# Performance work log

Hardware: AMD Instinct MI355X
Metric: run time of the kernel (lower is better)

The kernel has to match this reference:

```python
import jax, jax.numpy as jnp
import numpy as np

B, N, C, H = 64, 500, 128, 256
EPS = 1e-5


def _bn(x, g, b):
    # BatchNorm1d in training mode: biased batch statistics
    m = jnp.mean(x, axis=0)
    v = jnp.mean((x - m) ** 2, axis=0)
    return g * (x - m) * jax.lax.rsqrt(v + EPS) + b


def _lin(x, w, b):
    return x @ w.T + b


def setup_inputs() -> dict:
    key = jax.random.key(0)
    ks = jax.random.split(key, 16)

    def w(k, shape, s=0.05):
        return (s * jax.random.normal(k, shape)).astype(jnp.float32)

    return {
        'l2_xyz': jax.random.uniform(ks[0], (B, 3, N), dtype=jnp.float32),
        'l2_points': jax.random.normal(ks[1], (B, C, N), dtype=jnp.float32),
        'l3_points': jax.random.normal(ks[2], (B, C), dtype=jnp.float32),
        'temp': jax.random.uniform(ks[3], (B, 1, N), dtype=jnp.float32) * 400.0,
        'fc_res0_w': w(ks[4], (H, H)), 'fc_res0_b': jnp.zeros((H,), jnp.float32),
        'bn_res0_g': jnp.ones((H,), jnp.float32), 'bn_res0_b': jnp.zeros((H,), jnp.float32),
        'fc_res1_w': w(ks[5], (H, H)), 'fc_res1_b': jnp.zeros((H,), jnp.float32),
        'bn_res1_g': jnp.ones((H,), jnp.float32), 'bn_res1_b': jnp.zeros((H,), jnp.float32),
        'fc_res2_w': w(ks[6], (H, H)), 'fc_res2_b': jnp.zeros((H,), jnp.float32),
        'bn_res2_g': jnp.ones((H,), jnp.float32), 'bn_res2_b': jnp.zeros((H,), jnp.float32),
        'fc_lt1_w': w(ks[7], (H, H)), 'fc_lt1_b': jnp.zeros((H,), jnp.float32),
        'bn_lt1_g': jnp.ones((H,), jnp.float32), 'bn_lt1_b': jnp.zeros((H,), jnp.float32),
        'fc_lt4_w': w(ks[8], (1, H)), 'fc_lt4_b': jnp.zeros((1,), jnp.float32),
    }


def reference(l2_xyz, l2_points, l3_points, temp,
              fc_res0_w, fc_res0_b, bn_res0_g, bn_res0_b,
              fc_res1_w, fc_res1_b, bn_res1_g, bn_res1_b,
              fc_res2_w, fc_res2_b, bn_res2_g, bn_res2_b,
              fc_lt1_w, fc_lt1_b, bn_lt1_g, bn_lt1_b,
              fc_lt4_w, fc_lt4_b):
    point = jnp.transpose(l2_xyz, (0, 2, 1))    # [B,N,3]
    data = jnp.transpose(l2_points, (0, 2, 1))  # [B,N,C]

    # square_distance(point, point), then abs + sqrt
    s = jnp.sum(point * point, axis=-1)  # [B,N]
    sq = s[:, :, None] + s[:, None, :] - 2.0 * jnp.einsum('bik,bjk->bij', point, point)
    dist = jnp.sqrt(jnp.abs(sq))  # [B,N,N]

    # distance-band edge set as a mask (torch.where -> variable edge list)
    mask = ((dist > 0.19) & (dist < 0.21)).astype(data.dtype)  # [B,N,N]
    counts = jnp.maximum(jnp.sum(mask, axis=(1, 2)), 1.0)      # [B] edges per batch

    # per-channel average of data[b,i,c]*data[b,j,c] over edges (b,i,j).
    # Identical math to the torch take/index_add channel loop over corr_matrix,
    # without materializing the [B,C,N,N] outer-product tensor.
    t = jnp.einsum('bij,bjc->bic', mask, data)                  # [B,N,C]
    correlation = jnp.einsum('bic,bic->bc', t, data) / counts[:, None]  # [B,C]

    sa4 = l3_points.reshape(B, C)
    c = jnp.concatenate([correlation, sa4], axis=1)  # [B,256]

    h = jax.nn.relu(_bn(_lin(c, fc_res0_w, fc_res0_b), bn_res0_g, bn_res0_b))
    h = jax.nn.relu(_bn(_lin(h, fc_res1_w, fc_res1_b), bn_res1_g, bn_res1_b))
    h = jax.nn.relu(_bn(_lin(h, fc_res2_w, fc_res2_b), bn_res2_g, bn_res2_b))
    h = jax.nn.relu(_bn(_lin(h, fc_lt1_w, fc_lt1_b), bn_lt1_g, bn_lt1_b))
    tc = _lin(h, fc_lt4_w, fc_lt4_b).squeeze(-1)  # [B]

    tsys = jnp.mean(temp, axis=2).squeeze(-1)     # [B]
    return (tc, tsys, l2_points, correlation)
```

## Files before the change

### kernel.cpp

```cpp
#include <hip/hip_runtime.h>

#define NB 64
#define NP 500
#define NC 128
#define NH 256
#define EPS_BN 1e-5f

#define SEGS 8
#define CAPE 1024

#define EDGE_OFF 0
#define CNT_OFF (NB * SEGS * CAPE)
#define CT_OFF (CNT_OFF + 512)

#define OUT_PTS_OFF 128
#define OUT_CORR_OFF 4096128
#define TOTAL_F4 1024000

#define SCAN_BLKS 512
#define MISC_END 576
#define K1_COPY 1024
#define K1_GRID (MISC_END + K1_COPY)

typedef __attribute__((ext_vector_type(8))) short short8b;
typedef __attribute__((ext_vector_type(4))) float f32x4;

__device__ __forceinline__ short bfh(float f) {
  return (short)(__builtin_bit_cast(unsigned, f) >> 16);
}
__device__ __forceinline__ float bff(short h) {
  return __builtin_bit_cast(float, ((unsigned)(unsigned short)h) << 16);
}

__global__ __launch_bounds__(256) void k1_scan_misc_copy(
    const float* __restrict__ xyz,
    const float* __restrict__ temp,
    const float* __restrict__ l3,
    const float* __restrict__ pts,
    float* __restrict__ out,
    float* __restrict__ ws) {
  const int blk = blockIdx.x;
  const int tid = threadIdx.x;

  if (blk < SCAN_BLKS) {
    const int b = blk >> 3;
    const int jt = blk & 7;
    __shared__ float4 pt[NP];
    __shared__ int lcnt;
    if (tid == 0) lcnt = 0;
    const float* xr = xyz + b * 1500;
    for (int idx = tid; idx < NP; idx += 256) {
      float x = xr[idx], y = xr[500 + idx], z = xr[1000 + idx];
      pt[idx] = make_float4(x, y, z, x * x + y * y + z * z);
    }
    __syncthreads();

    const int j0 = jt * 63;
    const int j1 = (j0 + 63 < NP) ? j0 + 63 : NP;
    const int i0 = tid;
    const int i1 = tid + 256;
    float4 p0 = pt[i0];
    float4 p1 = (i1 < NP) ? pt[i1] : make_float4(0.f, 0.f, 0.f, 0.f);
    int* eseg = (int*)ws + EDGE_OFF + (b * SEGS + jt) * CAPE;

    for (int j = j0; j < j1; ++j) {
      float4 q = pt[j];
      if (i0 < j) {
        float sq = p0.w + q.w - 2.f * (p0.x * q.x + p0.y * q.y + p0.z * q.z);
        float d = sqrtf(fabsf(sq));
        if (d > 0.19f && d < 0.21f) {
          int e = atomicAdd(&lcnt, 1);
          if (e < CAPE) eseg[e] = (i0 << 16) | j;
        }
      }
      if (i1 < j) {
        float sq = p1.w + q.w - 2.f * (p1.x * q.x + p1.y * q.y + p1.z * q.z);
        float d = sqrtf(fabsf(sq));
        if (d > 0.19f && d < 0.21f) {
          int e = atomicAdd(&lcnt, 1);
          if (e < CAPE) eseg[e] = (i1 << 16) | j;
        }
      }
    }
    __syncthreads();
    if (tid == 0) {
      int c = lcnt < CAPE ? lcnt : CAPE;
      ((int*)ws)[CNT_OFF + b * SEGS + jt] = c;
    }
  } else if (blk < MISC_END) {
    const int b = blk - SCAN_BLKS;
    float sum = 0.f;
    for (int i = tid; i < NP; i += 256) sum += temp[b * NP + i];
    for (int off = 32; off; off >>= 1) sum += __shfl_xor(sum, off);
    __shared__ float wsum[4];
    if ((tid & 63) == 0) wsum[tid >> 6] = sum;
    __syncthreads();
    if (tid == 0)
      out[64 + b] = (wsum[0] + wsum[1] + wsum[2] + wsum[3]) * (1.f / 500.f);
    if (tid < NC) ws[CT_OFF + (NC + tid) * 64 + b] = l3[b * NC + tid];
  } else {
    const int cb = blk - MISC_END;
    const float4* src = (const float4*)pts;
    float4* dst = (float4*)(out + OUT_PTS_OFF);
    for (int idx = cb * 256 + tid; idx < TOTAL_F4; idx += K1_COPY * 256)
      dst[idx] = src[idx];
  }
}

__global__ __launch_bounds__(256) void k2_corr(
    const float* __restrict__ data,
    float* __restrict__ out,
    float* __restrict__ ws) {
  const int blk = blockIdx.x;
  const int tid = threadIdx.x;
  const int b = blk >> 3;
  const int c0 = (blk & 7) * 16;
  __shared__ float dT[NP * 20];
  __shared__ float corrp[16];
  if (tid < 16) corrp[tid] = 0.f;

  const float4* in4 = (const float4*)(data + (size_t)b * 64000 + c0 * 500);
  for (int idx = tid; idx < 2000; idx += 256) {
    float4 v = in4[idx];
    int c = idx / 125;
    int j = (idx - c * 125) * 4;
    dT[(j + 0) * 20 + c] = v.x;
    dT[(j + 1) * 20 + c] = v.y;
    dT[(j + 2) * 20 + c] = v.z;
    dT[(j + 3) * 20 + c] = v.w;
  }
  __syncthreads();

  const int quad = tid & 3;
  const int slot = tid >> 2;
  float4 acc = make_float4(0.f, 0.f, 0.f, 0.f);
  const int* cnts = (const int*)ws + CNT_OFF + b * SEGS;
  int Etot = 0;
  for (int seg = 0; seg < SEGS; ++seg) {
    int E = cnts[seg];
    Etot += E;
    const int* eseg = (const int*)ws + EDGE_OFF + (b * SEGS + seg) * CAPE;
    for (int e = slot; e < E; e += 64) {
      int ij = eseg[e];
      int i = ij >> 16, j = ij & 0xffff;
      const float4 a = *(const float4*)(dT + i * 20 + quad * 4);
      const float4 c4 = *(const float4*)(dT + j * 20 + quad * 4);
      acc.x += a.x * c4.x;
      acc.y += a.y * c4.y;
      acc.z += a.z * c4.z;
      acc.w += a.w * c4.w;
    }
  }
  for (int off = 4; off < 64; off <<= 1) {
    acc.x += __shfl_xor(acc.x, off);
    acc.y += __shfl_xor(acc.y, off);
    acc.z += __shfl_xor(acc.z, off);
    acc.w += __shfl_xor(acc.w, off);
  }
  if ((tid & 63) < 4) {
    atomicAdd(&corrp[quad * 4 + 0], acc.x);
    atomicAdd(&corrp[quad * 4 + 1], acc.y);
    atomicAdd(&corrp[quad * 4 + 2], acc.z);
    atomicAdd(&corrp[quad * 4 + 3], acc.w);
  }
  __syncthreads();
  if (tid < 16) {
    float denom = fmaxf(2.f * (float)Etot, 1.f);
    float v = 2.f * corrp[tid] / denom;
    out[OUT_CORR_OFF + b * NC + c0 + tid] = v;
    ws[CT_OFF + (c0 + tid) * 64 + b] = v;
  }
}

__device__ __forceinline__ void gemm_layer(const float* xT, const float* W,
                                           f32x4 (&acc)[4][4], int wv,
                                           int l15, int lg) {
#pragma unroll
  for (int t = 0; t < 4; ++t)
#pragma unroll
    for (int n = 0; n < 4; ++n) acc[t][n] = (f32x4){0.f, 0.f, 0.f, 0.f};

  for (int s = 0; s < 8; ++s) {
    short8b bh[4], bl[4];
#pragma unroll
    for (int n = 0; n < 4; ++n) {
#pragma unroll
      for (int i = 0; i < 8; ++i) {
        float f = xT[(s * 32 + lg * 8 + i) * 64 + n * 16 + l15];
        short h = bfh(f);
        bh[n][i] = h;
        bl[n][i] = bfh(f - bff(h));
      }
    }
#pragma unroll
    for (int t = 0; t < 4; ++t) {
      const float* wr = W + (wv * 64 + t * 16 + l15) * 256 + s * 32 + lg * 8;
      float4 wa = *(const float4*)wr;
      float4 wb = *(const float4*)(wr + 4);
      short8b ah, al;
#pragma unroll
      for (int i = 0; i < 4; ++i) {
        float fa = ((const float*)&wa)[i];
        short ha = bfh(fa);
        ah[i] = ha;
        al[i] = bfh(fa - bff(ha));
        float fb = ((const float*)&wb)[i];
        short hb = bfh(fb);
        ah[4 + i] = hb;
        al[4 + i] = bfh(fb - bff(hb));
      }
#pragma unroll
      for (int n = 0; n < 4; ++n) {
        acc[t][n] = __builtin_amdgcn_mfma_f32_16x16x32_bf16(ah, bh[n],
                                                            acc[t][n], 0, 0, 0);
        acc[t][n] = __builtin_amdgcn_mfma_f32_16x16x32_bf16(ah, bl[n],
                                                            acc[t][n], 0, 0, 0);
        acc[t][n] = __builtin_amdgcn_mfma_f32_16x16x32_bf16(al, bh[n],
                                                            acc[t][n], 0, 0, 0);
      }
    }
  }
}

__global__ __launch_bounds__(256) void k3_mlp(
    const float* __restrict__ ws, const float* __restrict__ w0,
    const float* __restrict__ g0, const float* __restrict__ be0,
    const float* __restrict__ w1, const float* __restrict__ g1,
    const float* __restrict__ be1, const float* __restrict__ w2,
    const float* __restrict__ g2, const float* __restrict__ be2,
    const float* __restrict__ w3, const float* __restrict__ g3,
    const float* __restrict__ be3, const float* __restrict__ w4,
    const float* __restrict__ b4, float* __restrict__ out) {
  const int tid = threadIdx.x;
  const int lane = tid & 63;
  const int wv = tid >> 6;
  const int l15 = lane & 15;
  const int lg = lane >> 4;

  __shared__ __align__(16) float xT[NH * NB];
  __shared__ float tcl[NB];

  const float4* src = (const float4*)(ws + CT_OFF);
  float4* dst4 = (float4*)xT;
  for (int i = tid; i < NH * NB / 4; i += 256) dst4[i] = src[i];
  if (tid < NB) tcl[tid] = 0.f;
  __syncthreads();

  f32x4 acc[4][4];
  const float* Ws[4] = {w0, w1, w2, w3};
  const float* Gs[4] = {g0, g1, g2, g3};
  const float* Bs[4] = {be0, be1, be2, be3};

#pragma unroll
  for (int L = 0; L < 4; ++L) {
    gemm_layer(xT, Ws[L], acc, wv, l15, lg);
    __syncthreads();

    if (L < 3) {
#pragma unroll
      for (int t = 0; t < 4; ++t) {
#pragma unroll
        for (int r = 0; r < 4; ++r) {
          const int o = wv * 64 + t * 16 + lg * 4 + r;
          float s1 = acc[t][0][r] + acc[t][1][r] + acc[t][2][r] + acc[t][3][r];
          s1 += __shfl_xor(s1, 1);
          s1 += __shfl_xor(s1, 2);
          s1 += __shfl_xor(s1, 4);
          s1 += __shfl_xor(s1, 8);
          float m = s1 * (1.f / 64.f);
          float d0 = acc[t][0][r] - m, d1 = acc[t][1][r] - m;
          float d2 = acc[t][2][r] - m, d3 = acc[t][3][r] - m;
          float s2 = d0 * d0 + d1 * d1 + d2 * d2 + d3 * d3;
          s2 += __shfl_xor(s2, 1);
          s2 += __shfl_xor(s2, 2);
          s2 += __shfl_xor(s2, 4);
          s2 += __shfl_xor(s2, 8);
          float sc = Gs[L][o] * rsqrtf(s2 * (1.f / 64.f) + EPS_BN);
          float bo = Bs[L][o];
          xT[o * 64 + 0 * 16 + l15] = fmaxf(d0 * sc + bo, 0.f);
          xT[o * 64 + 1 * 16 + l15] = fmaxf(d1 * sc + bo, 0.f);
          xT[o * 64 + 2 * 16 + l15] = fmaxf(d2 * sc + bo, 0.f);
          xT[o * 64 + 3 * 16 + l15] = fmaxf(d3 * sc + bo, 0.f);
        }
      }
      __syncthreads();
    } else {
      float part[4] = {0.f, 0.f, 0.f, 0.f};
#pragma unroll
      for (int t = 0; t < 4; ++t) {
#pragma unroll
        for (int r = 0; r < 4; ++r) {
          const int o = wv * 64 + t * 16 + lg * 4 + r;
          float s1 = acc[t][0][r] + acc[t][1][r] + acc[t][2][r] + acc[t][3][r];
          s1 += __shfl_xor(s1, 1);
          s1 += __shfl_xor(s1, 2);
          s1 += __shfl_xor(s1, 4);
          s1 += __shfl_xor(s1, 8);
          float m = s1 * (1.f / 64.f);
          float d0 = acc[t][0][r] - m, d1 = acc[t][1][r] - m;
          float d2 = acc[t][2][r] - m, d3 = acc[t][3][r] - m;
          float s2 = d0 * d0 + d1 * d1 + d2 * d2 + d3 * d3;
          s2 += __shfl_xor(s2, 1);
          s2 += __shfl_xor(s2, 2);
          s2 += __shfl_xor(s2, 4);
          s2 += __shfl_xor(s2, 8);
          float sc = Gs[3][o] * rsqrtf(s2 * (1.f / 64.f) + EPS_BN);
          float bo = Bs[3][o];
          float w4o = w4[o];
          part[0] += fmaxf(d0 * sc + bo, 0.f) * w4o;
          part[1] += fmaxf(d1 * sc + bo, 0.f) * w4o;
          part[2] += fmaxf(d2 * sc + bo, 0.f) * w4o;
          part[3] += fmaxf(d3 * sc + bo, 0.f) * w4o;
        }
      }
#pragma unroll
      for (int n = 0; n < 4; ++n) {
        part[n] += __shfl_xor(part[n], 16);
        part[n] += __shfl_xor(part[n], 32);
      }
      if (lg == 0) {
#pragma unroll
        for (int n = 0; n < 4; ++n) atomicAdd(&tcl[n * 16 + l15], part[n]);
      }
      __syncthreads();
      if (tid < NB) out[tid] = b4[0] + tcl[tid];
    }
  }
}

extern "C" void kernel_launch(void* const* d_in, const int* in_sizes, int n_in,
                              void* d_out, int out_size, void* d_ws,
                              size_t ws_size, hipStream_t stream) {
  const float* xyz = (const float*)d_in[0];
  const float* pts = (const float*)d_in[1];
  const float* l3 = (const float*)d_in[2];
  const float* temp = (const float*)d_in[3];
  const float* w0 = (const float*)d_in[4];
  const float* g0 = (const float*)d_in[6];
  const float* be0 = (const float*)d_in[7];
  const float* w1 = (const float*)d_in[8];
  const float* g1 = (const float*)d_in[10];
  const float* be1 = (const float*)d_in[11];
  const float* w2 = (const float*)d_in[12];
  const float* g2 = (const float*)d_in[14];
  const float* be2 = (const float*)d_in[15];
  const float* w3 = (const float*)d_in[16];
  const float* g3 = (const float*)d_in[18];
  const float* be3 = (const float*)d_in[19];
  const float* w4 = (const float*)d_in[20];
  const float* b4 = (const float*)d_in[21];

  float* out = (float*)d_out;
  float* ws = (float*)d_ws;

  k1_scan_misc_copy<<<K1_GRID, 256, 0, stream>>>(xyz, temp, l3, pts, out, ws);
  k2_corr<<<512, 256, 0, stream>>>(pts, out, ws);
  k3_mlp<<<1, 256, 0, stream>>>(ws, w0, g0, be0, w1, g1, be1, w2, g2, be2, w3,
                                g3, be3, w4, b4, out);
}
```

Measured before the change: 199.4 us.

## Restructure MLP kernel: 512 threads, pre-split bf16 activations in LDS, prefetched weights

The single-block MLP kernel now runs 8 waves instead of 4, and each wave computes 32 output rows instead of 64. Activations are kept in LDS already split into bf16 high and low parts, in a padded batch-major layout. This allows vector 16-byte LDS loads in place of per-element float loads and repeated conversion. Each layer's weight slice is loaded into registers up front. The aim is to shorten the serial latency-bound MLP tail, at the cost of heavy register use (128 floats of weights per thread) and extra conversion work in the BN write-back.

New measurement: 185.6 us. 6.9% less time.

```diff
diff --git a/kernel.cpp b/kernel.cpp
--- a/kernel.cpp
+++ b/kernel.cpp
@@ -21,6 +21,8 @@
 #define MISC_END 576
 #define K1_COPY 1024
 #define K1_GRID (MISC_END + K1_COPY)
+
+#define XS 264
 
 typedef __attribute__((ext_vector_type(8))) short short8b;
 typedef __attribute__((ext_vector_type(4))) float f32x4;
@@ -172,57 +174,7 @@
   }
 }
 
-__device__ __forceinline__ void gemm_layer(const float* xT, const float* W,
-                                           f32x4 (&acc)[4][4], int wv,
-                                           int l15, int lg) {
-#pragma unroll
-  for (int t = 0; t < 4; ++t)
-#pragma unroll
-    for (int n = 0; n < 4; ++n) acc[t][n] = (f32x4){0.f, 0.f, 0.f, 0.f};
-
-  for (int s = 0; s < 8; ++s) {
-    short8b bh[4], bl[4];
-#pragma unroll
-    for (int n = 0; n < 4; ++n) {
-#pragma unroll
-      for (int i = 0; i < 8; ++i) {
-        float f = xT[(s * 32 + lg * 8 + i) * 64 + n * 16 + l15];
-        short h = bfh(f);
-        bh[n][i] = h;
-        bl[n][i] = bfh(f - bff(h));
-      }
-    }
-#pragma unroll
-    for (int t = 0; t < 4; ++t) {
-      const float* wr = W + (wv * 64 + t * 16 + l15) * 256 + s * 32 + lg * 8;
-      float4 wa = *(const float4*)wr;
-      float4 wb = *(const float4*)(wr + 4);
-      short8b ah, al;
-#pragma unroll
-      for (int i = 0; i < 4; ++i) {
-        float fa = ((const float*)&wa)[i];
-        short ha = bfh(fa);
-        ah[i] = ha;
-        al[i] = bfh(fa - bff(ha));
-        float fb = ((const float*)&wb)[i];
-        short hb = bfh(fb);
-        ah[4 + i] = hb;
-        al[4 + i] = bfh(fb - bff(hb));
-      }
-#pragma unroll
-      for (int n = 0; n < 4; ++n) {
-        acc[t][n] = __builtin_amdgcn_mfma_f32_16x16x32_bf16(ah, bh[n],
-                                                            acc[t][n], 0, 0, 0);
-        acc[t][n] = __builtin_amdgcn_mfma_f32_16x16x32_bf16(ah, bl[n],
-                                                            acc[t][n], 0, 0, 0);
-        acc[t][n] = __builtin_amdgcn_mfma_f32_16x16x32_bf16(al, bh[n],
-                                                            acc[t][n], 0, 0, 0);
-      }
-    }
-  }
-}
-
-__global__ __launch_bounds__(256) void k3_mlp(
+__global__ __launch_bounds__(512) void k3_mlp(
     const float* __restrict__ ws, const float* __restrict__ w0,
     const float* __restrict__ g0, const float* __restrict__ be0,
     const float* __restrict__ w1, const float* __restrict__ g1,
@@ -237,39 +189,92 @@
   const int l15 = lane & 15;
   const int lg = lane >> 4;
 
-  __shared__ __align__(16) float xT[NH * NB];
+  __shared__ unsigned short xh[NB * XS];
+  __shared__ unsigned short xl[NB * XS];
   __shared__ float tcl[NB];
 
-  const float4* src = (const float4*)(ws + CT_OFF);
-  float4* dst4 = (float4*)xT;
-  for (int i = tid; i < NH * NB / 4; i += 256) dst4[i] = src[i];
+  const float* cws = ws + CT_OFF;
+  for (int idx = tid; idx < NH * NB; idx += 512) {
+    int o = idx >> 6, b = idx & 63;
+    float f = cws[idx];
+    short h = bfh(f);
+    xh[b * XS + o] = (unsigned short)h;
+    xl[b * XS + o] = (unsigned short)bfh(f - bff(h));
+  }
   if (tid < NB) tcl[tid] = 0.f;
   __syncthreads();
 
-  f32x4 acc[4][4];
   const float* Ws[4] = {w0, w1, w2, w3};
   const float* Gs[4] = {g0, g1, g2, g3};
   const float* Bs[4] = {be0, be1, be2, be3};
 
 #pragma unroll
   for (int L = 0; L < 4; ++L) {
-    gemm_layer(xT, Ws[L], acc, wv, l15, lg);
+    const float* W = Ws[L];
+    float wreg[2][64];
+#pragma unroll
+    for (int tt = 0; tt < 2; ++tt) {
+      const float* wr = W + ((wv * 2 + tt) * 16 + l15) * 256 + lg * 8;
+#pragma unroll
+      for (int s = 0; s < 8; ++s) {
+        *(float4*)&wreg[tt][s * 8] = *(const float4*)(wr + s * 32);
+        *(float4*)&wreg[tt][s * 8 + 4] = *(const float4*)(wr + s * 32 + 4);
+      }
+    }
+
+    f32x4 acc[2][4];
+#pragma unroll
+    for (int tt = 0; tt < 2; ++tt)
+#pragma unroll
+      for (int n = 0; n < 4; ++n) acc[tt][n] = (f32x4){0.f, 0.f, 0.f, 0.f};
+
+#pragma unroll
+    for (int s = 0; s < 8; ++s) {
+      short8b bh[4], bl[4];
+#pragma unroll
+      for (int n = 0; n < 4; ++n) {
+        const int lidx = (n * 16 + l15) * XS + s * 32 + lg * 8;
+        bh[n] = *(const short8b*)(xh + lidx);
+        bl[n] = *(const short8b*)(xl + lidx);
+      }
+#pragma unroll
+      for (int tt = 0; tt < 2; ++tt) {
+        short8b ah, al;
+#pragma unroll
+        for (int i = 0; i < 8; ++i) {
+          float f = wreg[tt][s * 8 + i];
+          short h = bfh(f);
+          ah[i] = h;
+          al[i] = bfh(f - bff(h));
+        }
+#pragma unroll
+        for (int n = 0; n < 4; ++n) {
+          acc[tt][n] = __builtin_amdgcn_mfma_f32_16x16x32_bf16(
+              ah, bh[n], acc[tt][n], 0, 0, 0);
+          acc[tt][n] = __builtin_amdgcn_mfma_f32_16x16x32_bf16(
+              ah, bl[n], acc[tt][n], 0, 0, 0);
+          acc[tt][n] = __builtin_amdgcn_mfma_f32_16x16x32_bf16(
+              al, bh[n], acc[tt][n], 0, 0, 0);
+        }
+      }
+    }
     __syncthreads();
 
     if (L < 3) {
 #pragma unroll
-      for (int t = 0; t < 4; ++t) {
+      for (int tt = 0; tt < 2; ++tt) {
 #pragma unroll
         for (int r = 0; r < 4; ++r) {
-          const int o = wv * 64 + t * 16 + lg * 4 + r;
-          float s1 = acc[t][0][r] + acc[t][1][r] + acc[t][2][r] + acc[t][3][r];
+          const int o = (wv * 2 + tt) * 16 + lg * 4 + r;
+          float a0 = acc[tt][0][r], a1 = acc[tt][1][r];
+          float a2 = acc[tt][2][r], a3 = acc[tt][3][r];
+          float s1 = a0 + a1 + a2 + a3;
           s1 += __shfl_xor(s1, 1);
           s1 += __shfl_xor(s1, 2);
           s1 += __shfl_xor(s1, 4);
           s1 += __shfl_xor(s1, 8);
           float m = s1 * (1.f / 64.f);
-          float d0 = acc[t][0][r] - m, d1 = acc[t][1][r] - m;
-          float d2 = acc[t][2][r] - m, d3 = acc[t][3][r] - m;
+          float d0 = a0 - m, d1 = a1 - m, d2 = a2 - m, d3 = a3 - m;
           float s2 = d0 * d0 + d1 * d1 + d2 * d2 + d3 * d3;
           s2 += __shfl_xor(s2, 1);
           s2 += __shfl_xor(s2, 2);
@@ -277,28 +282,34 @@
           s2 += __shfl_xor(s2, 8);
           float sc = Gs[L][o] * rsqrtf(s2 * (1.f / 64.f) + EPS_BN);
           float bo = Bs[L][o];
-          xT[o * 64 + 0 * 16 + l15] = fmaxf(d0 * sc + bo, 0.f);
-          xT[o * 64 + 1 * 16 + l15] = fmaxf(d1 * sc + bo, 0.f);
-          xT[o * 64 + 2 * 16 + l15] = fmaxf(d2 * sc + bo, 0.f);
-          xT[o * 64 + 3 * 16 + l15] = fmaxf(d3 * sc + bo, 0.f);
+          float hv[4] = {fmaxf(d0 * sc + bo, 0.f), fmaxf(d1 * sc + bo, 0.f),
+                         fmaxf(d2 * sc + bo, 0.f), fmaxf(d3 * sc + bo, 0.f)};
+#pragma unroll
+          for (int n = 0; n < 4; ++n) {
+            short h = bfh(hv[n]);
+            xh[(n * 16 + l15) * XS + o] = (unsigned short)h;
+            xl[(n * 16 + l15) * XS + o] =
+                (unsigned short)bfh(hv[n] - bff(h));
+          }
         }
       }
       __syncthreads();
     } else {
       float part[4] = {0.f, 0.f, 0.f, 0.f};
 #pragma unroll
-      for (int t = 0; t < 4; ++t) {
+      for (int tt = 0; tt < 2; ++tt) {
 #pragma unroll
         for (int r = 0; r < 4; ++r) {
-          const int o = wv * 64 + t * 16 + lg * 4 + r;
-          float s1 = acc[t][0][r] + acc[t][1][r] + acc[t][2][r] + acc[t][3][r];
+          const int o = (wv * 2 + tt) * 16 + lg * 4 + r;
+          float a0 = acc[tt][0][r], a1 = acc[tt][1][r];
+          float a2 = acc[tt][2][r], a3 = acc[tt][3][r];
+          float s1 = a0 + a1 + a2 + a3;
           s1 += __shfl_xor(s1, 1);
           s1 += __shfl_xor(s1, 2);
           s1 += __shfl_xor(s1, 4);
           s1 += __shfl_xor(s1, 8);
           float m = s1 * (1.f / 64.f);
-          float d0 = acc[t][0][r] - m, d1 = acc[t][1][r] - m;
-          float d2 = acc[t][2][r] - m, d3 = acc[t][3][r] - m;
+          float d0 = a0 - m, d1 = a1 - m, d2 = a2 - m, d3 = a3 - m;
           float s2 = d0 * d0 + d1 * d1 + d2 * d2 + d3 * d3;
           s2 += __shfl_xor(s2, 1);
           s2 += __shfl_xor(s2, 2);
@@ -355,6 +366,6 @@
 
   k1_scan_misc_copy<<<K1_GRID, 256, 0, stream>>>(xyz, temp, l3, pts, out, ws);
   k2_corr<<<512, 256, 0, stream>>>(pts, out, ws);
-  k3_mlp<<<1, 256, 0, stream>>>(ws, w0, g0, be0, w1, g1, be1, w2, g2, be2, w3,
+  k3_mlp<<<1, 512, 0, stream>>>(ws, w0, g0, be0, w1, g1, be1, w2, g2, be2, w3,
                                 g3, be3, w4, b4, out);
 }
```

## Split single-block MLP into four per-layer 16-block MFMA kernel launches

Applied to the files above, without the earlier changes.

Replaces the one-block, four-layer MLP kernel with a per-layer kernel launched four times. Each launch uses 16 single-wave blocks, one per 16-output tile, and activations pass between layers through global workspace instead of LDS. The final layer atomically accumulates into the output, which is pre-seeded with the fc_lt4 bias in the first kernel. This spreads the weight loads and MFMA work across more compute units, but adds three extra kernel launches and global-memory round trips for the activations.

Measured after the change: 172.2 us. 13.6% less time.

```diff
diff --git a/kernel.cpp b/kernel.cpp
--- a/kernel.cpp
+++ b/kernel.cpp
@@ -12,6 +12,8 @@
 #define EDGE_OFF 0
 #define CNT_OFF (NB * SEGS * CAPE)
 #define CT_OFF (CNT_OFF + 512)
+#define H1_OFF (CT_OFF + NH * NB)
+#define H2_OFF (H1_OFF + NH * NB)
 
 #define OUT_PTS_OFF 128
 #define OUT_CORR_OFF 4096128
@@ -36,6 +38,7 @@
     const float* __restrict__ xyz,
     const float* __restrict__ temp,
     const float* __restrict__ l3,
+    const float* __restrict__ b4,
     const float* __restrict__ pts,
     float* __restrict__ out,
     float* __restrict__ ws) {
@@ -98,6 +101,7 @@
     if (tid == 0)
       out[64 + b] = (wsum[0] + wsum[1] + wsum[2] + wsum[3]) * (1.f / 500.f);
     if (tid < NC) ws[CT_OFF + (NC + tid) * 64 + b] = l3[b * NC + tid];
+    if (tid == 0) out[b] = b4[0];
   } else {
     const int cb = blk - MISC_END;
     const float4* src = (const float4*)pts;
@@ -172,14 +176,40 @@
   }
 }
 
-__device__ __forceinline__ void gemm_layer(const float* xT, const float* W,
-                                           f32x4 (&acc)[4][4], int wv,
-                                           int l15, int lg) {
-#pragma unroll
-  for (int t = 0; t < 4; ++t)
-#pragma unroll
-    for (int n = 0; n < 4; ++n) acc[t][n] = (f32x4){0.f, 0.f, 0.f, 0.f};
-
+__global__ __launch_bounds__(64) void lmfma(
+    const float* __restrict__ xT, const float* __restrict__ W,
+    const float* __restrict__ g, const float* __restrict__ be,
+    float* __restrict__ yT, const float* __restrict__ w4,
+    float* __restrict__ tc) {
+  const int lane = threadIdx.x;
+  const int l15 = lane & 15;
+  const int lg = lane >> 4;
+  const int ot = blockIdx.x;
+
+  short8b ah[8], al[8];
+  const float* wr = W + (ot * 16 + l15) * 256 + lg * 8;
+#pragma unroll
+  for (int s = 0; s < 8; ++s) {
+    float4 wa = *(const float4*)(wr + s * 32);
+    float4 wb = *(const float4*)(wr + s * 32 + 4);
+#pragma unroll
+    for (int i = 0; i < 4; ++i) {
+      float fa = ((const float*)&wa)[i];
+      short h = bfh(fa);
+      ah[s][i] = h;
+      al[s][i] = bfh(fa - bff(h));
+      float fb = ((const float*)&wb)[i];
+      h = bfh(fb);
+      ah[s][4 + i] = h;
+      al[s][4 + i] = bfh(fb - bff(h));
+    }
+  }
+
+  f32x4 acc[4];
+#pragma unroll
+  for (int n = 0; n < 4; ++n) acc[n] = (f32x4){0.f, 0.f, 0.f, 0.f};
+
+#pragma unroll
   for (int s = 0; s < 8; ++s) {
     short8b bh[4], bl[4];
 #pragma unroll
@@ -193,137 +223,74 @@
       }
     }
 #pragma unroll
-    for (int t = 0; t < 4; ++t) {
-      const float* wr = W + (wv * 64 + t * 16 + l15) * 256 + s * 32 + lg * 8;
-      float4 wa = *(const float4*)wr;
-      float4 wb = *(const float4*)(wr + 4);
-      short8b ah, al;
-#pragma unroll
-      for (int i = 0; i < 4; ++i) {
-        float fa = ((const float*)&wa)[i];
-        short ha = bfh(fa);
-        ah[i] = ha;
-        al[i] = bfh(fa - bff(ha));
-        float fb = ((const float*)&wb)[i];
-        short hb = bfh(fb);
-        ah[4 + i] = hb;
-        al[4 + i] = bfh(fb - bff(hb));
-      }
-#pragma unroll
-      for (int n = 0; n < 4; ++n) {
-        acc[t][n] = __builtin_amdgcn_mfma_f32_16x16x32_bf16(ah, bh[n],
-                                                            acc[t][n], 0, 0, 0);
-        acc[t][n] = __builtin_amdgcn_mfma_f32_16x16x32_bf16(ah, bl[n],
-                                                            acc[t][n], 0, 0, 0);
-        acc[t][n] = __builtin_amdgcn_mfma_f32_16x16x32_bf16(al, bh[n],
-                                                            acc[t][n], 0, 0, 0);
-      }
-    }
-  }
-}
-
-__global__ __launch_bounds__(256) void k3_mlp(
-    const float* __restrict__ ws, const float* __restrict__ w0,
-    const float* __restrict__ g0, const float* __restrict__ be0,
-    const float* __restrict__ w1, const float* __restrict__ g1,
-    const float* __restrict__ be1, const float* __restrict__ w2,
-    const float* __restrict__ g2, const float* __restrict__ be2,
-    const float* __restrict__ w3, const float* __restrict__ g3,
-    const float* __restrict__ be3, const float* __restrict__ w4,
-    const float* __restrict__ b4, float* __restrict__ out) {
-  const int tid = threadIdx.x;
-  const int lane = tid & 63;
-  const int wv = tid >> 6;
-  const int l15 = lane & 15;
-  const int lg = lane >> 4;
-
-  __shared__ __align__(16) float xT[NH * NB];
-  __shared__ float tcl[NB];
-
-  const float4* src = (const float4*)(ws + CT_OFF);
-  float4* dst4 = (float4*)xT;
-  for (int i = tid; i < NH * NB / 4; i += 256) dst4[i] = src[i];
-  if (tid < NB) tcl[tid] = 0.f;
-  __syncthreads();
-
-  f32x4 acc[4][4];
-  const float* Ws[4] = {w0, w1, w2, w3};
-  const float* Gs[4] = {g0, g1, g2, g3};
-  const float* Bs[4] = {be0, be1, be2, be3};
-
-#pragma unroll
-  for (int L = 0; L < 4; ++L) {
-    gemm_layer(xT, Ws[L], acc, wv, l15, lg);
-    __syncthreads();
-
-    if (L < 3) {
-#pragma unroll
-      for (int t = 0; t < 4; ++t) {
-#pragma unroll
-        for (int r = 0; r < 4; ++r) {
-          const int o = wv * 64 + t * 16 + lg * 4 + r;
-          float s1 = acc[t][0][r] + acc[t][1][r] + acc[t][2][r] + acc[t][3][r];
-          s1 += __shfl_xor(s1, 1);
-          s1 += __shfl_xor(s1, 2);
-          s1 += __shfl_xor(s1, 4);
-          s1 += __shfl_xor(s1, 8);
-          float m = s1 * (1.f / 64.f);
-          float d0 = acc[t][0][r] - m, d1 = acc[t][1][r] - m;
-          float d2 = acc[t][2][r] - m, d3 = acc[t][3][r] - m;
-          float s2 = d0 * d0 + d1 * d1 + d2 * d2 + d3 * d3;
-          s2 += __shfl_xor(s2, 1);
-          s2 += __shfl_xor(s2, 2);
-          s2 += __shfl_xor(s2, 4);
-          s2 += __shfl_xor(s2, 8);
-          float sc = Gs[L][o] * rsqrtf(s2 * (1.f / 64.f) + EPS_BN);
-          float bo = Bs[L][o];
-          xT[o * 64 + 0 * 16 + l15] = fmaxf(d0 * sc + bo, 0.f);
-          xT[o * 64 + 1 * 16 + l15] = fmaxf(d1 * sc + bo, 0.f);
-          xT[o * 64 + 2 * 16 + l15] = fmaxf(d2 * sc + bo, 0.f);
-          xT[o * 64 + 3 * 16 + l15] = fmaxf(d3 * sc + bo, 0.f);
-        }
-      }
-      __syncthreads();
-    } else {
-      float part[4] = {0.f, 0.f, 0.f, 0.f};
-#pragma unroll
-      for (int t = 0; t < 4; ++t) {
-#pragma unroll
-        for (int r = 0; r < 4; ++r) {
-          const int o = wv * 64 + t * 16 + lg * 4 + r;
-          float s1 = acc[t][0][r] + acc[t][1][r] + acc[t][2][r] + acc[t][3][r];
-          s1 += __shfl_xor(s1, 1);
-          s1 += __shfl_xor(s1, 2);
-          s1 += __shfl_xor(s1, 4);
-          s1 += __shfl_xor(s1, 8);
-          float m = s1 * (1.f / 64.f);
-          float d0 = acc[t][0][r] - m, d1 = acc[t][1][r] - m;
-          float d2 = acc[t][2][r] - m, d3 = acc[t][3][r] - m;
-          float s2 = d0 * d0 + d1 * d1 + d2 * d2 + d3 * d3;
-          s2 += __shfl_xor(s2, 1);
-          s2 += __shfl_xor(s2, 2);
-          s2 += __shfl_xor(s2, 4);
-          s2 += __shfl_xor(s2, 8);
-          float sc = Gs[3][o] * rsqrtf(s2 * (1.f / 64.f) + EPS_BN);
-          float bo = Bs[3][o];
-          float w4o = w4[o];
-          part[0] += fmaxf(d0 * sc + bo, 0.f) * w4o;
-          part[1] += fmaxf(d1 * sc + bo, 0.f) * w4o;
-          part[2] += fmaxf(d2 * sc + bo, 0.f) * w4o;
-          part[3] += fmaxf(d3 * sc + bo, 0.f) * w4o;
-        }
-      }
-#pragma unroll
-      for (int n = 0; n < 4; ++n) {
-        part[n] += __shfl_xor(part[n], 16);
-        part[n] += __shfl_xor(part[n], 32);
-      }
-      if (lg == 0) {
-#pragma unroll
-        for (int n = 0; n < 4; ++n) atomicAdd(&tcl[n * 16 + l15], part[n]);
-      }
-      __syncthreads();
-      if (tid < NB) out[tid] = b4[0] + tcl[tid];
+    for (int n = 0; n < 4; ++n) {
+      acc[n] = __builtin_amdgcn_mfma_f32_16x16x32_bf16(ah[s], bh[n], acc[n],
+                                                       0, 0, 0);
+      acc[n] = __builtin_amdgcn_mfma_f32_16x16x32_bf16(ah[s], bl[n], acc[n],
+                                                       0, 0, 0);
+      acc[n] = __builtin_amdgcn_mfma_f32_16x16x32_bf16(al[s], bh[n], acc[n],
+                                                       0, 0, 0);
+    }
+  }
+
+  if (!w4) {
+#pragma unroll
+    for (int r = 0; r < 4; ++r) {
+      const int o = ot * 16 + lg * 4 + r;
+      float a0 = acc[0][r], a1 = acc[1][r], a2 = acc[2][r], a3 = acc[3][r];
+      float s1 = a0 + a1 + a2 + a3;
+      s1 += __shfl_xor(s1, 1);
+      s1 += __shfl_xor(s1, 2);
+      s1 += __shfl_xor(s1, 4);
+      s1 += __shfl_xor(s1, 8);
+      float m = s1 * (1.f / 64.f);
+      float d0 = a0 - m, d1 = a1 - m, d2 = a2 - m, d3 = a3 - m;
+      float s2 = d0 * d0 + d1 * d1 + d2 * d2 + d3 * d3;
+      s2 += __shfl_xor(s2, 1);
+      s2 += __shfl_xor(s2, 2);
+      s2 += __shfl_xor(s2, 4);
+      s2 += __shfl_xor(s2, 8);
+      float sc = g[o] * rsqrtf(s2 * (1.f / 64.f) + EPS_BN);
+      float bo = be[o];
+      yT[o * 64 + 0 * 16 + l15] = fmaxf(d0 * sc + bo, 0.f);
+      yT[o * 64 + 1 * 16 + l15] = fmaxf(d1 * sc + bo, 0.f);
+      yT[o * 64 + 2 * 16 + l15] = fmaxf(d2 * sc + bo, 0.f);
+      yT[o * 64 + 3 * 16 + l15] = fmaxf(d3 * sc + bo, 0.f);
+    }
+  } else {
+    float part[4] = {0.f, 0.f, 0.f, 0.f};
+#pragma unroll
+    for (int r = 0; r < 4; ++r) {
+      const int o = ot * 16 + lg * 4 + r;
+      float a0 = acc[0][r], a1 = acc[1][r], a2 = acc[2][r], a3 = acc[3][r];
+      float s1 = a0 + a1 + a2 + a3;
+      s1 += __shfl_xor(s1, 1);
+      s1 += __shfl_xor(s1, 2);
+      s1 += __shfl_xor(s1, 4);
+      s1 += __shfl_xor(s1, 8);
+      float m = s1 * (1.f / 64.f);
+      float d0 = a0 - m, d1 = a1 - m, d2 = a2 - m, d3 = a3 - m;
+      float s2 = d0 * d0 + d1 * d1 + d2 * d2 + d3 * d3;
+      s2 += __shfl_xor(s2, 1);
+      s2 += __shfl_xor(s2, 2);
+      s2 += __shfl_xor(s2, 4);
+      s2 += __shfl_xor(s2, 8);
+      float sc = g[o] * rsqrtf(s2 * (1.f / 64.f) + EPS_BN);
+      float bo = be[o];
+      float w4o = w4[o];
+      part[0] += fmaxf(d0 * sc + bo, 0.f) * w4o;
+      part[1] += fmaxf(d1 * sc + bo, 0.f) * w4o;
+      part[2] += fmaxf(d2 * sc + bo, 0.f) * w4o;
+      part[3] += fmaxf(d3 * sc + bo, 0.f) * w4o;
+    }
+#pragma unroll
+    for (int n = 0; n < 4; ++n) {
+      part[n] += __shfl_xor(part[n], 16);
+      part[n] += __shfl_xor(part[n], 32);
+    }
+    if (lg == 0) {
+#pragma unroll
+      for (int n = 0; n < 4; ++n) atomicAdd(&tc[n * 16 + l15], part[n]);
     }
   }
 }
@@ -352,9 +319,15 @@
 
   float* out = (float*)d_out;
   float* ws = (float*)d_ws;
-
-  k1_scan_misc_copy<<<K1_GRID, 256, 0, stream>>>(xyz, temp, l3, pts, out, ws);
+  float* cT = ws + CT_OFF;
+  float* hA = ws + H1_OFF;
+  float* hB = ws + H2_OFF;
+
+  k1_scan_misc_copy<<<K1_GRID, 256, 0, stream>>>(xyz, temp, l3, b4, pts, out,
+                                                 ws);
   k2_corr<<<512, 256, 0, stream>>>(pts, out, ws);
-  k3_mlp<<<1, 256, 0, stream>>>(ws, w0, g0, be0, w1, g1, be1, w2, g2, be2, w3,
-                                g3, be3, w4, b4, out);
-}
+  lmfma<<<16, 64, 0, stream>>>(cT, w0, g0, be0, hA, nullptr, nullptr);
+  lmfma<<<16, 64, 0, stream>>>(hA, w1, g1, be1, hB, nullptr, nullptr);
+  lmfma<<<16, 64, 0, stream>>>(hB, w2, g2, be2, hA, nullptr, nullptr);
+  lmfma<<<16, 64, 0, stream>>>(hA, w3, g3, be3, nullptr, w4, out);
+}
```
